# Optimization experiments

Measured on AMD Instinct MI355X. Metric: run time of the kernel, lower is better.

Reference implementation:

```python
import jax, jax.numpy as jnp
import numpy as np

jax.config.update("jax_enable_x64", True)  # hash math needs int64, matching torch .long()

IN_DIM = 3
N_LEVELS = 16
F = 2
B = 1.38
BASE = 16
T = 524309  # nextprime(2**19)
PS = np.array([1, 19349663, 83492791], dtype=np.int64)  # first in_dim primes
ENTRIES_NUM = np.array([[int(BASE * B ** i)] * IN_DIM for i in range(N_LEVELS)], dtype=np.int64)
ENTRIES_CNT = np.prod(ENTRIES_NUM, axis=1)
ENTRIES_SIZE = (1.0 / (ENTRIES_NUM - 1)).astype(np.float32)
ENTRIES_SUM = np.cumsum(ENTRIES_CNT)
S = int(np.argmax(ENTRIES_CNT > T))  # start_hash = 6
H = N_LEVELS - S                     # 10 hashed levels
K = 2 ** IN_DIM                      # 8 cube corners
DENSE_SIZE = int(ENTRIES_SUM[S - 1])  # 822944
# binary corner offsets, MSB-first (matches the source's bit loop)
OFFSETS = np.array([[(i >> (IN_DIM - 1 - d)) & 1 for d in range(IN_DIM)] for i in range(K)], dtype=np.float32)
# row-major strides for dense levels: prod of trailing resolutions per dim
STRIDES = np.stack([np.prod(ENTRIES_NUM[:S, i + 1:], axis=1) for i in range(IN_DIM)], axis=1)  # (S,3)
BASE_OFF = np.concatenate([np.zeros(1, np.int64), ENTRIES_SUM[:S - 1]])  # per-level offset into dense
BOUNDS = np.array([[0., 0., 0.], [1., 1., 1.]], dtype=np.float32)


def setup_inputs() -> dict:
    key = jax.random.key(0)
    k1, k2, k3 = jax.random.split(key, 3)
    xyz = jax.random.uniform(k1, (2, 65536, 3), dtype=jnp.float32)
    dense = (jax.random.uniform(k2, (DENSE_SIZE, F), dtype=jnp.float32) * 2 - 1) * 1e-4
    hash_table = (jax.random.uniform(k3, (H, T, F), dtype=jnp.float32) * 2 - 1) * 1e-4
    return {"xyz": xyz, "dense": dense, "hash_table": hash_table}


def _forward(xyz, dense, hash_table):
    bash = xyz.shape
    x = xyz.reshape(-1, IN_DIM)
    N = x.shape[0]
    x = (x - BOUNDS[0]) / (BOUNDS[1] - BOUNDS[0])  # normalize to [0,1]
    flt = x[None] / jnp.asarray(ENTRIES_SIZE)[:, None]  # (L,N,3): coords in grid units
    intx = (flt[:, :, None] + jnp.asarray(OFFSETS)[None, None]).astype(jnp.int64)  # (L,N,K,3)
    intx = jnp.clip(intx, 0, jnp.asarray(ENTRIES_NUM)[:, None, None] - 1)
    off = flt - intx[:, :, 0].astype(flt.dtype)  # (L,N,3) fractional offset from corner 0
    # dense (non-hashed) levels: row-major linear index + level base offset
    ind_dense = (intx[:S] * jnp.asarray(STRIDES)[:, None, None, :]).sum(-1)  # (S,N,K)
    ind_dense = ind_dense + jnp.asarray(BASE_OFF)[:, None, None]
    # hashed levels: XOR of prime-multiplied coords, seeded with ones (as in source)
    ih = jnp.ones_like(intx[S:, ..., 0])
    for i in range(IN_DIM):
        ih = ih ^ (intx[S:, ..., i] * int(PS[i]))
    ih = ih % T  # (H,N,K)
    val_dense = dense[ind_dense]  # (S,N,K,F) gather
    val_hash = jnp.take_along_axis(hash_table, ih.reshape(H, -1)[..., None], axis=1).reshape(H, N, K, F)
    val = jnp.concatenate([val_dense, val_hash], axis=0)  # (L,N,K,F)
    o = jnp.asarray(OFFSETS)[None, None]  # (1,1,K,3)
    w = 1 - o + (2 * o - 1.0) * off[:, :, None]  # (L,N,K,3) per-dim lerp weights
    w = w[..., 0] * w[..., 1]  # NOTE: source multiplies only dims 0 and 1 (replicated faithfully)
    val = (w[..., None] * val).sum(-2)  # (L,N,F)
    val = jnp.transpose(val, (1, 0, 2)).reshape(N, N_LEVELS * F)  # (N, 32)
    out = jnp.concatenate([x, val], axis=-1)  # include_input -> (N, 35)
    return out.reshape(*bash[:-1], out.shape[-1])


def reference(xyz, dense, hash_table):
    return _forward(xyz, dense, hash_table)
```

## Files before the change

kernel.cpp:

```cpp
#include <hip/hip_runtime.h>
#include <cstdint>


namespace {
constexpr int NLEV   = 16;
constexpr int SDENSE = 6;
constexpr uint64_t T_HASH = 524309ull;

typedef float f2v __attribute__((ext_vector_type(2)));
typedef float f4v __attribute__((ext_vector_type(4)));
struct __attribute__((packed, aligned(8))) F4A8 { f4v v; };
static_assert(sizeof(F4A8) == 16, "");

__constant__ int c_res[NLEV] = {16,22,30,42,58,80,110,152,210,290,400,553,763,1053,1453,2005};
__constant__ float c_es[NLEV] = {
    (float)(1.0/15.0),  (float)(1.0/21.0),  (float)(1.0/29.0),  (float)(1.0/41.0),
    (float)(1.0/57.0),  (float)(1.0/79.0),  (float)(1.0/109.0), (float)(1.0/151.0),
    (float)(1.0/209.0), (float)(1.0/289.0), (float)(1.0/399.0), (float)(1.0/552.0),
    (float)(1.0/762.0), (float)(1.0/1052.0),(float)(1.0/1452.0),(float)(1.0/2004.0)
};
__constant__ int c_base[SDENSE] = {0, 4096, 14744, 41744, 115832, 310944};
}

__device__ __forceinline__ void level_eval(
    const float2* __restrict__ dense,
    const float2* __restrict__ hashtab,
    float x0, float x1, float x2, int l,
    float& acc0, float& acc1)
{
    int   res = c_res[l];
    float es  = c_es[l];
    float f0 = x0 / es;
    float f1 = x1 / es;
    float f2 = x2 / es;
    int nm1 = res - 1;

    int i00 = min(max((int)f0, 0), nm1);
    int i01 = min(max((int)f1, 0), nm1);
    int i02 = min(max((int)f2, 0), nm1);
    int i10 = min(max((int)(f0 + 1.0f), 0), nm1);
    int i11 = min(max((int)(f1 + 1.0f), 0), nm1);
    int i12 = min(max((int)(f2 + 1.0f), 0), nm1);
    (void)i12;

    float off0 = f0 - (float)i00;
    float off1 = f1 - (float)i01;
    float w0a = 1.0f - off0, w0b = off0;
    float w1a = 1.0f - off1, w1b = off1;
    float wxy0 = w0a * w1a, wxy1 = w0a * w1b, wxy2 = w0b * w1a, wxy3 = w0b * w1b;

    acc0 = 0.0f; acc1 = 0.0f;

    if (l < SDENSE) {
        int s0   = res * res;
        int base = c_base[l];
        int A0 = i00 * s0,  A1 = i10 * s0;
        int B0 = i01 * res, B1 = i11 * res;
        int  zlo    = min(i02, nm1 - 1);
        bool lowSel = (i02 == zlo);
        #pragma unroll
        for (int k = 0; k < 4; ++k) {
            int idx = ((k & 2) ? A1 : A0) + ((k & 1) ? B1 : B0) + zlo + base;
            f4v v = reinterpret_cast<const F4A8*>(dense + idx)->v;
            float lo0 = lowSel ? v.x : v.z;
            float lo1 = lowSel ? v.y : v.w;
            float w = (k & 2) ? ((k & 1) ? wxy3 : wxy2) : ((k & 1) ? wxy1 : wxy0);
            acc0 += w * (lo0 + v.z);
            acc1 += w * (lo1 + v.w);
        }
    } else {
        uint64_t a0 = (uint64_t)(uint32_t)i00;
        uint64_t a1 = (uint64_t)(uint32_t)i10;
        uint64_t b0 = (uint64_t)(uint32_t)i01 * 19349663ull;
        uint64_t b1 = (uint64_t)(uint32_t)i11 * 19349663ull;
        uint64_t cz0 = (uint64_t)(uint32_t)i02 * 83492791ull;
        uint64_t cz1 = (uint64_t)(uint32_t)min(i02 + 1, nm1) * 83492791ull;
        uint32_t rowbase = (uint32_t)(l - SDENSE) * (uint32_t)T_HASH;
        #pragma unroll
        for (int k = 0; k < 4; ++k) {
            uint64_t hb = 1ull ^ ((k & 2) ? a1 : a0) ^ ((k & 1) ? b1 : b0);
            uint32_t idx0 = rowbase + (uint32_t)((hb ^ cz0) % T_HASH);
            uint32_t idx1 = rowbase + (uint32_t)((hb ^ cz1) % T_HASH);
            float2 v0 = hashtab[idx0];
            float2 v1 = hashtab[idx1];
            float w = (k & 2) ? ((k & 1) ? wxy3 : wxy2) : ((k & 1) ? wxy1 : wxy0);
            acc0 += w * (v0.x + v1.x);
            acc1 += w * (v0.y + v1.y);
        }
    }
}

__global__ __launch_bounds__(256) void hashgrid_level(
    const float*  __restrict__ xyz,
    const float2* __restrict__ dense,
    const float2* __restrict__ hashtab,
    float2*       __restrict__ ws,
    int npts)
{
    int b = blockIdx.x;
    int x = b & 7;
    int s = b >> 3;
    int level, chunk;
    if (s < 768) {
        int g = 768 * x + s;
        level = 4 + (g >> 9);
        chunk = g & 511;
    } else {
        int h = 256 * x + (s - 768);
        level = h >> 9;
        chunk = h & 511;
    }
    int n0 = chunk << 8;
    int t  = threadIdx.x;

    __shared__ float sxyz[768];
    sxyz[t      ] = xyz[3 * n0 + t      ];
    sxyz[t + 256] = xyz[3 * n0 + t + 256];
    sxyz[t + 512] = xyz[3 * n0 + t + 512];
    __syncthreads();
    float x0 = sxyz[3 * t], x1 = sxyz[3 * t + 1], x2 = sxyz[3 * t + 2];

    float acc0, acc1;
    level_eval(dense, hashtab, x0, x1, x2, level, acc0, acc1);

    f2v val = {acc0, acc1};
    __builtin_nontemporal_store(val, (f2v*)(ws + (size_t)level * npts + n0 + t));
}

__global__ __launch_bounds__(256) void gather_out(
    const float*  __restrict__ xyz,
    const float2* __restrict__ ws,
    float*        __restrict__ out,
    int npts)
{
    __shared__ __align__(16) float tile[256 * 35];
    int t  = threadIdx.x;
    int n0 = blockIdx.x << 8;
    int n  = n0 + t;

    #pragma unroll
    for (int j = 0; j < 3; ++j) {
        int pos = t + (j << 8);
        float v = xyz[3 * n0 + pos];
        int pt = pos / 3, dim = pos - 3 * pt;
        tile[pt * 35 + dim] = v;
    }
    #pragma unroll
    for (int l = 0; l < NLEV; ++l) {
        f2v v = __builtin_nontemporal_load((const f2v*)(ws + (size_t)l * npts + n));
        tile[t * 35 + 3 + 2 * l] = v.x;
        tile[t * 35 + 4 + 2 * l] = v.y;
    }
    __syncthreads();

    const f4v* src = (const f4v*)tile;
    f4v* dst = (f4v*)(out + (size_t)n0 * 35);
    #pragma unroll
    for (int i = 0; i < 9; ++i) {
        int idx = t + (i << 8);
        if (idx < 2240) __builtin_nontemporal_store(src[idx], dst + idx);
    }
}

__global__ __launch_bounds__(256) void hashgrid_mono(
    const float*  __restrict__ xyz,
    const float2* __restrict__ dense,
    const float2* __restrict__ hashtab,
    float*        __restrict__ out,
    int npts)
{
    int tid = blockIdx.x * 256 + threadIdx.x;
    int l = tid & (NLEV - 1);
    int n = tid >> 4;
    if (n >= npts) return;

    float x0 = xyz[3*n+0], x1 = xyz[3*n+1], x2 = xyz[3*n+2];
    float acc0, acc1;
    level_eval(dense, hashtab, x0, x1, x2, l, acc0, acc1);

    float* o = out + (size_t)n * 35;
    if (l == 0) { o[0] = x0; o[1] = x1; o[2] = x2; }
    o[3 + 2*l] = acc0;
    o[4 + 2*l] = acc1;
}

extern "C" void kernel_launch(void* const* d_in, const int* in_sizes, int n_in,
                              void* d_out, int out_size, void* d_ws, size_t ws_size,
                              hipStream_t stream) {
    const float*  xyz     = (const float*)d_in[0];
    const float2* dense   = (const float2*)d_in[1];
    const float2* hashtab = (const float2*)d_in[2];
    float* out = (float*)d_out;

    int npts = in_sizes[0] / 3;
    size_t ws_need = (size_t)NLEV * (size_t)npts * sizeof(float2);

    if (npts == 131072 && ws_size >= ws_need) {
        float2* ws = (float2*)d_ws;
        hashgrid_level<<<8192, 256, 0, stream>>>(xyz, dense, hashtab, ws, npts);
        gather_out<<<npts / 256, 256, 0, stream>>>(xyz, ws, out, npts);
    } else {
        int total  = npts * NLEV;
        int blocks = (total + 255) / 256;
        hashgrid_mono<<<blocks, 256, 0, stream>>>(xyz, dense, hashtab, out, npts);
    }
}
```

Measured before the change: 155.4 us.

## Rebalance level-chunk work across XCDs and route hash loads through L2

Replaces the fixed per-block level/chunk mapping with a cost-weighted partition. Each XCD gets a contiguous range of level-ordered chunks, split by precomputed cut points, and each block loops over a small span of chunks. The point is to keep hashed levels for the same table on the same XCD so their L2 stays warm, and to even out work between the costlier hashed levels and the dense ones. Hash-table reads now use relaxed agent-scope atomic loads, which steers them to L2 instead of per-CU L1. The looped blocks add extra syncs, the uneven chunk counts per block can cause tail imbalance, and the atomic loads may cost more per access.

```diff
diff --git a/kernel.cpp b/kernel.cpp
--- a/kernel.cpp
+++ b/kernel.cpp
@@ -20,6 +20,16 @@
     (float)(1.0/762.0), (float)(1.0/1052.0),(float)(1.0/1452.0),(float)(1.0/2004.0)
 };
 __constant__ int c_base[SDENSE] = {0, 4096, 14744, 41744, 115832, 310944};
+
+__constant__ int c_order[NLEV] = {6,7,8,9,10,11,12,13,14,15,5,4,3,2,1,0};
+__constant__ int c_cut[9] = {0, 762, 1523, 2285, 3046, 3808, 4570, 5472, 8192};
+}
+
+__device__ __forceinline__ f2v ld_l2_f2(const float2* p) {
+    unsigned long long u = __hip_atomic_load(
+        (const unsigned long long*)p, __ATOMIC_RELAXED, __HIP_MEMORY_SCOPE_AGENT);
+    union { unsigned long long u; f2v f; } cv; cv.u = u;
+    return cv.f;
 }
 
 __device__ __forceinline__ void level_eval(
@@ -40,8 +50,6 @@
     int i02 = min(max((int)f2, 0), nm1);
     int i10 = min(max((int)(f0 + 1.0f), 0), nm1);
     int i11 = min(max((int)(f1 + 1.0f), 0), nm1);
-    int i12 = min(max((int)(f2 + 1.0f), 0), nm1);
-    (void)i12;
 
     float off0 = f0 - (float)i00;
     float off1 = f1 - (float)i01;
@@ -81,8 +89,8 @@
             uint64_t hb = 1ull ^ ((k & 2) ? a1 : a0) ^ ((k & 1) ? b1 : b0);
             uint32_t idx0 = rowbase + (uint32_t)((hb ^ cz0) % T_HASH);
             uint32_t idx1 = rowbase + (uint32_t)((hb ^ cz1) % T_HASH);
-            float2 v0 = hashtab[idx0];
-            float2 v1 = hashtab[idx1];
+            f2v v0 = ld_l2_f2(hashtab + idx0);
+            f2v v1 = ld_l2_f2(hashtab + idx1);
             float w = (k & 2) ? ((k & 1) ? wxy3 : wxy2) : ((k & 1) ? wxy1 : wxy0);
             acc0 += w * (v0.x + v1.x);
             acc1 += w * (v0.y + v1.y);
@@ -100,31 +108,31 @@
     int b = blockIdx.x;
     int x = b & 7;
     int s = b >> 3;
-    int level, chunk;
-    if (s < 768) {
-        int g = 768 * x + s;
-        level = 4 + (g >> 9);
-        chunk = g & 511;
-    } else {
-        int h = 256 * x + (s - 768);
-        level = h >> 9;
-        chunk = h & 511;
-    }
-    int n0 = chunk << 8;
+    int lo = c_cut[x];
+    int L  = c_cut[x + 1] - lo;
+    int c0 = lo + ((s * L) >> 10);
+    int c1 = lo + (((s + 1) * L) >> 10);
     int t  = threadIdx.x;
 
     __shared__ float sxyz[768];
-    sxyz[t      ] = xyz[3 * n0 + t      ];
-    sxyz[t + 256] = xyz[3 * n0 + t + 256];
-    sxyz[t + 512] = xyz[3 * n0 + t + 512];
-    __syncthreads();
-    float x0 = sxyz[3 * t], x1 = sxyz[3 * t + 1], x2 = sxyz[3 * t + 2];
-
-    float acc0, acc1;
-    level_eval(dense, hashtab, x0, x1, x2, level, acc0, acc1);
-
-    f2v val = {acc0, acc1};
-    __builtin_nontemporal_store(val, (f2v*)(ws + (size_t)level * npts + n0 + t));
+
+    for (int c = c0; c < c1; ++c) {
+        int level = c_order[c >> 9];
+        int n0    = (c & 511) << 8;
+
+        __syncthreads();
+        sxyz[t      ] = xyz[3 * n0 + t      ];
+        sxyz[t + 256] = xyz[3 * n0 + t + 256];
+        sxyz[t + 512] = xyz[3 * n0 + t + 512];
+        __syncthreads();
+        float x0 = sxyz[3 * t], x1 = sxyz[3 * t + 1], x2 = sxyz[3 * t + 2];
+
+        float acc0, acc1;
+        level_eval(dense, hashtab, x0, x1, x2, level, acc0, acc1);
+
+        f2v val = {acc0, acc1};
+        __builtin_nontemporal_store(val, (f2v*)(ws + (size_t)level * npts + n0 + t));
+    }
 }
 
 __global__ __launch_bounds__(256) void gather_out(
```

Measured after the change: 175.9 us. +13.2%, slower.
